# Kernel optimization log

Hardware: AMD Instinct MI355X
Metric: run time of the kernel (lower is better)

Reference implementation:

```python
import jax, jax.numpy as jnp
import numpy as np
from jax import lax

C = 32          # channel_num
DG = 8          # deformable_groups
K = 9           # 3x3 deformable kernel taps
B, H, W = 4, 192, 192


def conv2d(x, w, b, pad):
    y = lax.conv_general_dilated(x, w, (1, 1), [(pad, pad), (pad, pad)],
                                 dimension_numbers=("NCHW", "OIHW", "NCHW"))
    return y + b[None, :, None, None]


def deform_conv2d(x, offset, mask, w, b):
    """Modulated deformable conv v2, 3x3 kernel, stride 1, pad 1, dilation 1.

    x:      [B, C, H, W]
    offset: [B, 2*DG*K, H, W]  laid out as cat(o1, o2): first DG*K = dy, next = dx
    mask:   [B, DG*K, H, W]    (already sigmoided)
    w:      [Cout, C, 3, 3], b: [Cout]
    """
    Bn, Cn, Hn, Wn = x.shape
    Cg = Cn // DG
    off = offset.reshape(Bn, 2, DG, K, Hn, Wn)
    dy, dx = off[:, 0], off[:, 1]                     # [B, DG, K, H, W]
    m = mask.reshape(Bn, DG, K, Hn, Wn)

    ky = jnp.repeat(jnp.arange(3) - 1, 3).astype(x.dtype)  # [K]
    kx = jnp.tile(jnp.arange(3) - 1, 3).astype(x.dtype)    # [K]
    iy = jnp.arange(Hn, dtype=x.dtype)
    ix = jnp.arange(Wn, dtype=x.dtype)
    py = dy + ky[None, None, :, None, None] + iy[None, None, None, :, None]
    px = dx + kx[None, None, :, None, None] + ix[None, None, None, None, :]

    y0 = jnp.floor(py)
    x0 = jnp.floor(px)
    wy = py - y0    # frac weights
    wx = px - x0

    x_flat = x.reshape(Bn, DG, Cg, Hn * Wn)

    def gather(yc, xc):
        valid = (yc >= 0) & (yc < Hn) & (xc >= 0) & (xc < Wn)
        yi = jnp.clip(yc, 0, Hn - 1).astype(jnp.int32)
        xi = jnp.clip(xc, 0, Wn - 1).astype(jnp.int32)
        idx = (yi * Wn + xi).reshape(Bn, DG, 1, K * Hn * Wn)
        v = jnp.take_along_axis(x_flat, jnp.broadcast_to(idx, (Bn, DG, Cg, K * Hn * Wn)), axis=3)
        v = v.reshape(Bn, DG, Cg, K, Hn, Wn)
        return v * valid[:, :, None].astype(x.dtype)

    v00 = gather(y0, x0)
    v01 = gather(y0, x0 + 1)
    v10 = gather(y0 + 1, x0)
    v11 = gather(y0 + 1, x0 + 1)
    wyb = wy[:, :, None]  # [B, DG, 1, K, H, W]
    wxb = wx[:, :, None]
    sampled = ((1 - wyb) * (1 - wxb) * v00 + (1 - wyb) * wxb * v01
               + wyb * (1 - wxb) * v10 + wyb * wxb * v11)
    sampled = sampled * m[:, :, None]                 # modulate
    sampled = sampled.reshape(Bn, Cn, K, Hn, Wn)      # DG*Cg == C, contiguous
    out = jnp.einsum('oik,bikhw->bohw', w.reshape(w.shape[0], Cn, K), sampled)
    return out + b[None, :, None, None]


def setup_inputs() -> dict:
    key = jax.random.key(0)
    ks = jax.random.split(key, 14)
    f = lambda k, shp, s=1.0: jax.random.normal(k, shp, dtype=jnp.float32) * s
    return {
        "img_ref": f(ks[0], (B, C, H, W)),
        "img": f(ks[1], (B, C, H, W)),
        "conv1_w": f(ks[2], (C, 2 * C, 1, 1), 0.05),
        "conv1_b": f(ks[3], (C,), 0.05),
        "conv2a_w": f(ks[4], (C, C, 3, 3), 0.05),
        "conv2a_b": f(ks[5], (C,), 0.05),
        "conv2b_w": f(ks[6], (C, C, 3, 3), 0.05),
        "conv2b_b": f(ks[7], (C,), 0.05),
        "off_w": f(ks[8], (3 * DG * K, C, 3, 3), 0.01),
        "off_b": f(ks[9], (3 * DG * K,), 0.01),
        "dcn_w": f(ks[10], (C, C, 3, 3), 0.05),
        "dcn_b": f(ks[11], (C,), 0.05),
    }


def reference(img_ref, img, conv1_w, conv1_b, conv2a_w, conv2a_b,
              conv2b_w, conv2b_b, off_w, off_b, dcn_w, dcn_b):
    img_cat = conv2d(jnp.concatenate([img_ref, img], axis=1), conv1_w, conv1_b, 0)
    feat = conv2d(conv2d(img_cat, conv2a_w, conv2a_b, 1), conv2b_w, conv2b_b, 1)
    # DCNv2Pack: offsets/mask from feat, deformable sampling on img
    co = conv2d(feat, off_w, off_b, 1)                # [B, 3*DG*K, H, W]
    o1, o2, mask = jnp.split(co, 3, axis=1)
    offset = jnp.concatenate([o1, o2], axis=1)
    mask = jax.nn.sigmoid(mask)
    return deform_conv2d(img, offset, mask, dcn_w, dcn_b)
```

## Files before the change

kernel.cpp:

```cpp
#include <hip/hip_runtime.h>

#define Hc   192
#define Wc   192
#define HWc  (Hc * Wc)
#define NPIX (4 * HWc)
#define Hp   194
#define Wp   256
#define PLANE (Hp * Wp)

typedef float f32x4 __attribute__((ext_vector_type(4)));
typedef float f32x2 __attribute__((ext_vector_type(2)));
typedef __bf16 bf16x8 __attribute__((ext_vector_type(8)));
typedef unsigned short u16;
typedef unsigned int u32;

#define WF_BO    0
#define WF_B1    224
#define WF_B2A   256
#define WF_B2B   288
#define WF_BD    320
#define FR1_U    0
#define FRA_U    2048
#define FRB_U    11264
#define FRO_U    20480
#define FRD_U    84992
#define FRAG_U_TOT 94208
#define FRAG_BYTE 1408
#define T0_BYTE  (FRAG_BYTE + FRAG_U_TOT * 2)
#define T1_BYTE  (T0_BYTE + NPIX * 32 * 2)
#define IMG_BYTE (T1_BYTE + NPIX * 32 * 2)
#define IMG_SZ   ((size_t)4 * 8 * PLANE * 4 * 2)

__device__ __forceinline__ u16 f2bf(float f) {
    u32 u = __float_as_uint(f);
    u32 r = u + 0x7fffu + ((u >> 16) & 1u);
    return (u16)(r >> 16);
}
__device__ __forceinline__ float bf2f(u16 v) {
    return __uint_as_float(((u32)v) << 16);
}
__device__ __forceinline__ u32 cvtpk(float a, float b) {
    u32 r;
    asm("v_cvt_pk_bf16_f32 %0, %1, %2" : "=v"(r) : "v"(a), "v"(b));
    return r;
}
__device__ __forceinline__ f32x2 unpk(u32 h) {
    return f32x2{__uint_as_float(h << 16), __uint_as_float(h & 0xffff0000u)};
}

__global__ __launch_bounds__(256) void prep_k(
    const float* __restrict__ w1,  const float* __restrict__ b1,
    const float* __restrict__ w2a, const float* __restrict__ b2a,
    const float* __restrict__ w2b, const float* __restrict__ b2b,
    const float* __restrict__ wo,  const float* __restrict__ bo,
    const float* __restrict__ wd,  const float* __restrict__ bd,
    float* __restrict__ wsf, u16* __restrict__ frag)
{
    int i = blockIdx.x * 256 + threadIdx.x;
    if (i < 224)      { wsf[WF_BO + i]  = (i < 216) ? bo[i] : 0.f; return; }
    if (i < 256)      { wsf[WF_B1  + i - 224] = b1[i - 224];  return; }
    if (i < 288)      { wsf[WF_B2A + i - 256] = b2a[i - 256]; return; }
    if (i < 320)      { wsf[WF_B2B + i - 288] = b2b[i - 288]; return; }
    if (i < 352)      { wsf[WF_BD  + i - 320] = bd[i - 320];  return; }
    int fi = i - 352;
    if (fi < 2048) {
        int s = fi >> 10, l = (fi >> 3) & 63, j = fi & 7;
        int nt = (fi >> 9) & 1;
        int o = nt * 16 + (l & 15);
        int ci = s * 32 + ((l >> 4) << 3) + j;
        frag[FR1_U + fi] = f2bf(w1[o * 64 + ci]);
        return;
    }
    fi -= 2048;
    if (fi < 9216) {
        int s = fi / 1024, r = fi - s * 1024;
        int nt = r >> 9, l = (r >> 3) & 63, j = r & 7;
        int o = nt * 16 + (l & 15);
        int ci = ((l >> 4) << 3) + j;
        frag[FRA_U + fi] = f2bf(w2a[(o * 32 + ci) * 9 + s]);
        return;
    }
    fi -= 9216;
    if (fi < 9216) {
        int s = fi / 1024, r = fi - s * 1024;
        int nt = r >> 9, l = (r >> 3) & 63, j = r & 7;
        int o = nt * 16 + (l & 15);
        int ci = ((l >> 4) << 3) + j;
        frag[FRB_U + fi] = f2bf(w2b[(o * 32 + ci) * 9 + s]);
        return;
    }
    fi -= 9216;
    if (fi < 64512) {
        int s = fi / 7168, r = fi - s * 7168;
        int nt = r >> 9, l = (r >> 3) & 63, j = r & 7;
        int o = nt * 16 + (l & 15);
        int ci = ((l >> 4) << 3) + j;
        frag[FRO_U + fi] = f2bf((o < 216) ? wo[(o * 32 + ci) * 9 + s] : 0.f);
        return;
    }
    fi -= 64512;
    if (fi < 9216) {
        int k = fi / 1024, r = fi - k * 1024;
        int nt = r >> 9, l = (r >> 3) & 63, j = r & 7;
        int o = nt * 16 + (l & 15);
        int ci = ((l >> 4) << 3) + j;
        frag[FRD_U + fi] = f2bf(wd[o * 288 + ci * 9 + k]);
        return;
    }
}

template <int WM, int WN, int MF, int NF, int COUT, int NTILES, int KS, int MODE, bool CHL, bool DUMP>
__global__ __launch_bounds__(256) void conv_mfma_k(
    const void* __restrict__ s0v, const void* __restrict__ s1v,
    const u16* __restrict__ wfrag, const float* __restrict__ bias,
    u16* __restrict__ y, u16* __restrict__ dump)
{
    constexpr int M_BLK = WM * MF * 16;
    constexpr int ITERS = M_BLK / 64;
    const int tid = threadIdx.x, lane = tid & 63, wv = tid >> 6;
    const int wm = wv / WN, wn = wv % WN;
    const int m0 = blockIdx.x * M_BLK;
    const int b = m0 / HWc, hwb = m0 - b * HWc;
    const int rm = wm * MF * 16, cn = wn * NF * 16;

    __shared__ uint4 At4[M_BLK * 4];

    int pxA[ITERS], hA[ITERS], wA[ITERS], kgA[ITERS];
#pragma unroll
    for (int it = 0; it < ITERS; ++it) {
        int st = it * 256 + tid;
        int rowl = ((st >> 6) << 4) | (st & 15);
        kgA[it] = (st >> 4) & 3;
        pxA[it] = rowl;
        int hwp = hwb + rowl;
        hA[it] = hwp / Wc;
        wA[it] = hwp - hA[it] * Wc;
    }

    f32x4 acc[MF][NF];
#pragma unroll
    for (int mf = 0; mf < MF; ++mf)
#pragma unroll
        for (int nf = 0; nf < NF; ++nf)
            acc[mf][nf] = f32x4{0.f, 0.f, 0.f, 0.f};

    const u16* srcB = (const u16*)s0v;
    const float* f0 = (const float*)s0v;
    const float* f1 = (const float*)s1v;

    for (int s = 0; s < KS; ++s) {
        if (MODE == 1) {
            int dy = s / 3 - 1, dx = s - (s / 3) * 3 - 1;
            int d = dy * Wc + dx;
#pragma unroll
            for (int it = 0; it < ITERS; ++it) {
                bool valid = ((unsigned)(hA[it] + dy) < (unsigned)Hc) &&
                             ((unsigned)(wA[it] + dx) < (unsigned)Wc);
                uint4 v = {0u, 0u, 0u, 0u};
                if (valid)
                    v = *(const uint4*)(srcB + ((size_t)(m0 + pxA[it] + d)) * 32 + kgA[it] * 8);
                At4[it * 256 + tid] = v;
            }
        } else {
            const float* fs = (s == 0) ? f0 : f1;
#pragma unroll
            for (int it = 0; it < ITERS; ++it) {
                const float* pl = fs + ((size_t)b * 32 + kgA[it] * 8) * HWc + (hwb + pxA[it]);
                u32 p0, p1, p2, p3;
                {
                    u32 a0 = f2bf(pl[0 * HWc]), a1 = f2bf(pl[1 * HWc]);
                    u32 a2 = f2bf(pl[2 * HWc]), a3 = f2bf(pl[3 * HWc]);
                    u32 a4 = f2bf(pl[4 * HWc]), a5 = f2bf(pl[5 * HWc]);
                    u32 a6 = f2bf(pl[6 * HWc]), a7 = f2bf(pl[7 * HWc]);
                    p0 = a0 | (a1 << 16); p1 = a2 | (a3 << 16);
                    p2 = a4 | (a5 << 16); p3 = a6 | (a7 << 16);
                }
                uint4 v = {p0, p1, p2, p3};
                if (DUMP && s == 1) {
                    size_t base = (((size_t)(b * 8 + kgA[it] * 2)) * PLANE
                                   + (size_t)(hA[it] + 1) * Wp + (wA[it] + 1)) * 4;
                    *(uint2*)(dump + base) = uint2{p0, p1};
                    *(uint2*)(dump + base + (size_t)PLANE * 4) = uint2{p2, p3};
                }
                At4[it * 256 + tid] = v;
            }
        }
        __syncthreads();

        bf16x8 aF[MF];
#pragma unroll
        for (int mf = 0; mf < MF; ++mf)
            aF[mf] = __builtin_bit_cast(bf16x8, At4[((rm >> 4) + mf) * 64 + lane]);
#pragma unroll
        for (int nf = 0; nf < NF; ++nf) {
            bf16x8 bF = __builtin_bit_cast(
                bf16x8,
                *(const uint4*)(wfrag + (((size_t)s * NTILES + wn * NF + nf) * 64 + lane) * 8));
#pragma unroll
            for (int mf = 0; mf < MF; ++mf)
                acc[mf][nf] = __builtin_amdgcn_mfma_f32_16x16x32_bf16(aF[mf], bF, acc[mf][nf], 0, 0, 0);
        }
        __syncthreads();
    }

#pragma unroll
    for (int nf = 0; nf < NF; ++nf) {
        int o = cn + nf * 16 + (lane & 15);
        float bs = bias[o];
#pragma unroll
        for (int mf = 0; mf < MF; ++mf) {
#pragma unroll
            for (int r = 0; r < 4; ++r) {
                int m = m0 + rm + mf * 16 + ((lane >> 4) << 2) + r;
                float val = acc[mf][nf][r] + bs;
                y[(size_t)m * COUT + o] = f2bf(val);
            }
        }
    }
}

__global__ __launch_bounds__(256, 4) void offdcn_k(
    const u16* __restrict__ t0,
    const u16* __restrict__ imgp,
    const u16* __restrict__ wfragO,
    const u16* __restrict__ wfragD,
    const float* __restrict__ biasO,
    const float* __restrict__ biasD,
    float* __restrict__ out)
{
    const int tid = threadIdx.x, lane = tid & 63, wv = tid >> 6;
    const int bid = blockIdx.x;
    const int swz = (bid & 7) * 288 + (bid >> 3);
    const int m0 = swz * 64;
    const int b = m0 / HWc, hwb = m0 - b * HWc;
    const int h0 = hwb / Wc, w0 = hwb - h0 * Wc;

    __shared__ u16 pool[224 * 66];

    {
        u16* xt = pool;
#pragma unroll
        for (int it = 0; it < 4; ++it) {
            int t = it * 256 + tid;
            if (t < 792) {
                int s = t >> 2, c = t & 3;
                int ry = s / 66, cx = s - ry * 66;
                int row = h0 + ry - 1, col = w0 + cx - 1;
                uint4 v = {0u, 0u, 0u, 0u};
                if (((unsigned)row < (unsigned)Hc) && ((unsigned)col < (unsigned)Wc))
                    v = *(const uint4*)(t0 + ((size_t)(b * HWc + row * Wc + col)) * 32 + c * 8);
                *(uint4*)(xt + (size_t)t * 8) = v;
            }
        }
    }
    __syncthreads();

    const int wm = wv >> 1, wn = wv & 1;
    const int rm = wm * 32, cn = wn * 112;
    f32x4 acc[2][7];
#pragma unroll
    for (int mf = 0; mf < 2; ++mf)
#pragma unroll
        for (int nf = 0; nf < 7; ++nf)
            acc[mf][nf] = f32x4{0.f, 0.f, 0.f, 0.f};
    {
        const u16* xt = pool;
        const int r0 = rm + (lane & 15);
        const int kg8 = (lane >> 4) * 8;
#pragma unroll
        for (int kyi = 0; kyi < 3; ++kyi) {
#pragma unroll
            for (int kxi = 0; kxi < 3; ++kxi) {
                const int s9 = kyi * 3 + kxi;
                bf16x8 aF0 = __builtin_bit_cast(bf16x8,
                    *(const uint4*)(xt + (size_t)(kyi * 66 + r0 + kxi) * 32 + kg8));
                bf16x8 aF1 = __builtin_bit_cast(bf16x8,
                    *(const uint4*)(xt + (size_t)(kyi * 66 + r0 + 16 + kxi) * 32 + kg8));
#pragma unroll
                for (int nf = 0; nf < 7; ++nf) {
                    bf16x8 bF = __builtin_bit_cast(
                        bf16x8,
                        *(const uint4*)(wfragO + (((size_t)s9 * 14 + wn * 7 + nf) * 64 + lane) * 8));
                    acc[0][nf] = __builtin_amdgcn_mfma_f32_16x16x32_bf16(aF0, bF, acc[0][nf], 0, 0, 0);
                    acc[1][nf] = __builtin_amdgcn_mfma_f32_16x16x32_bf16(aF1, bF, acc[1][nf], 0, 0, 0);
                }
            }
        }
    }
    __syncthreads();

    u16* co_s = pool;
#pragma unroll
    for (int nf = 0; nf < 7; ++nf) {
        const int o = cn + nf * 16 + (lane & 15);
        const float bs = biasO[o];
        const bool sig = (o >= 144);
#pragma unroll
        for (int mf = 0; mf < 2; ++mf) {
            const int mb = rm + mf * 16 + ((lane >> 4) << 2);
            float v0 = acc[mf][nf][0] + bs, v1 = acc[mf][nf][1] + bs;
            float v2 = acc[mf][nf][2] + bs, v3 = acc[mf][nf][3] + bs;
            if (sig) {
                v0 = __builtin_amdgcn_rcpf(1.f + __builtin_amdgcn_exp2f(-v0 * 1.44269504f));
                v1 = __builtin_amdgcn_rcpf(1.f + __builtin_amdgcn_exp2f(-v1 * 1.44269504f));
                v2 = __builtin_amdgcn_rcpf(1.f + __builtin_amdgcn_exp2f(-v2 * 1.44269504f));
                v3 = __builtin_amdgcn_rcpf(1.f + __builtin_amdgcn_exp2f(-v3 * 1.44269504f));
            }
            *(u32*)&co_s[o * 66 + mb]     = cvtpk(v0, v1);
            *(u32*)&co_s[o * 66 + mb + 2] = cvtpk(v2, v3);
        }
    }
    __syncthreads();

    {
        const int kg = lane >> 4;
        const int pixb = wv * 16 + (lane & 15);
        const int hw = hwb + pixb;
        const int hh = hw / Wc;
        const int wwp = hw - hh * Wc;

        f32x4 acc0 = {0.f, 0.f, 0.f, 0.f};
        f32x4 acc1 = {0.f, 0.f, 0.f, 0.f};

#pragma unroll 1
        for (int kb = 0; kb < 9; kb += 3) {
            float w4[3][2][4];
            uint2 cc[3][2][4];

#pragma unroll
            for (int t = 0; t < 3; ++t) {
                const int k = kb + t;
                const int kyi = k / 3, kxi = k - kyi * 3;
#pragma unroll
                for (int dgi = 0; dgi < 2; ++dgi) {
                    const int dg = 2 * kg + dgi;
                    const int offch = dg * 9 + k;
                    float dy = bf2f(co_s[offch * 66 + pixb]);
                    float dx = bf2f(co_s[(72 + offch) * 66 + pixb]);
                    float m  = bf2f(co_s[(144 + offch) * 66 + pixb]);

                    float py = dy + (float)(hh + kyi - 1);
                    float px = dx + (float)(wwp + kxi - 1);
                    float y0f = floorf(py), x0f = floorf(px);
                    float wy = py - y0f, wx = px - x0f;
                    int y0 = (int)y0f, x0 = (int)x0f;

                    int yA = min(max(y0 + 1, 0), 193);
                    int yB = min(max(y0 + 2, 0), 193);
                    int xA = min(max(x0 + 1, 0), 193);
                    int xB = min(max(x0 + 2, 0), 193);

                    float w1y = 1.f - wy, w1x = 1.f - wx;
                    w4[t][dgi][0] = w1y * w1x * m;
                    w4[t][dgi][1] = w1y * wx  * m;
                    w4[t][dgi][2] = wy  * w1x * m;
                    w4[t][dgi][3] = wy  * wx  * m;

                    const u16* pp = imgp + ((size_t)(b * 8 + dg)) * PLANE * 4;
                    cc[t][dgi][0] = *(const uint2*)(pp + (size_t)((yA << 8) + xA) * 4);
                    cc[t][dgi][1] = *(const uint2*)(pp + (size_t)((yA << 8) + xB) * 4);
                    cc[t][dgi][2] = *(const uint2*)(pp + (size_t)((yB << 8) + xA) * 4);
                    cc[t][dgi][3] = *(const uint2*)(pp + (size_t)((yB << 8) + xB) * 4);
                }
            }

#pragma unroll
            for (int t = 0; t < 3; ++t) {
                const int k = kb + t;
                u32 pk[4];
#pragma unroll
                for (int dgi = 0; dgi < 2; ++dgi) {
                    f32x2 sA = unpk(cc[t][dgi][0].x) * w4[t][dgi][0]
                             + unpk(cc[t][dgi][1].x) * w4[t][dgi][1]
                             + unpk(cc[t][dgi][2].x) * w4[t][dgi][2]
                             + unpk(cc[t][dgi][3].x) * w4[t][dgi][3];
                    f32x2 sB = unpk(cc[t][dgi][0].y) * w4[t][dgi][0]
                             + unpk(cc[t][dgi][1].y) * w4[t][dgi][1]
                             + unpk(cc[t][dgi][2].y) * w4[t][dgi][2]
                             + unpk(cc[t][dgi][3].y) * w4[t][dgi][3];
                    pk[dgi * 2 + 0] = cvtpk(sA.x, sA.y);
                    pk[dgi * 2 + 1] = cvtpk(sB.x, sB.y);
                }

                bf16x8 aF = __builtin_bit_cast(bf16x8, uint4{pk[0], pk[1], pk[2], pk[3]});
                bf16x8 bF0 = __builtin_bit_cast(bf16x8,
                    *(const uint4*)(wfragD + ((size_t)(k * 2 + 0) * 64 + lane) * 8));
                bf16x8 bF1 = __builtin_bit_cast(bf16x8,
                    *(const uint4*)(wfragD + ((size_t)(k * 2 + 1) * 64 + lane) * 8));
                acc0 = __builtin_amdgcn_mfma_f32_16x16x32_bf16(aF, bF0, acc0, 0, 0, 0);
                acc1 = __builtin_amdgcn_mfma_f32_16x16x32_bf16(aF, bF1, acc1, 0, 0, 0);
            }
        }

        const int hw0 = hwb + wv * 16 + ((lane >> 4) << 2);
        float* ob = out + (size_t)b * 32 * HWc;
        const int oL = lane & 15;
        const float bs0 = biasD[oL], bs1 = biasD[16 + oL];
        f32x4 o0 = {acc0[0] + bs0, acc0[1] + bs0, acc0[2] + bs0, acc0[3] + bs0};
        f32x4 o1 = {acc1[0] + bs1, acc1[1] + bs1, acc1[2] + bs1, acc1[3] + bs1};
        *(f32x4*)(ob + (size_t)oL * HWc + hw0) = o0;
        *(f32x4*)(ob + (size_t)(16 + oL) * HWc + hw0) = o1;
    }
}

extern "C" void kernel_launch(void* const* d_in, const int* in_sizes, int n_in,
                              void* d_out, int out_size, void* d_ws, size_t ws_size,
                              hipStream_t stream) {
    const float* img_ref  = (const float*)d_in[0];
    const float* img      = (const float*)d_in[1];
    const float* conv1_w  = (const float*)d_in[2];
    const float* conv1_b  = (const float*)d_in[3];
    const float* conv2a_w = (const float*)d_in[4];
    const float* conv2a_b = (const float*)d_in[5];
    const float* conv2b_w = (const float*)d_in[6];
    const float* conv2b_b = (const float*)d_in[7];
    const float* off_w    = (const float*)d_in[8];
    const float* off_b    = (const float*)d_in[9];
    const float* dcn_w    = (const float*)d_in[10];
    const float* dcn_b    = (const float*)d_in[11];

    float* wsf = (float*)d_ws;
    u16* frag = (u16*)((char*)d_ws + FRAG_BYTE);
    u16* t0   = (u16*)((char*)d_ws + T0_BYTE);
    u16* t1   = (u16*)((char*)d_ws + T1_BYTE);
    u16* imgp = (u16*)((char*)d_ws + IMG_BYTE);
    float* out = (float*)d_out;

    hipMemsetAsync(imgp, 0, IMG_SZ, stream);

    prep_k<<<370, 256, 0, stream>>>(conv1_w, conv1_b, conv2a_w, conv2a_b,
                                    conv2b_w, conv2b_b, off_w, off_b,
                                    dcn_w, dcn_b, wsf, frag);

    conv_mfma_k<4, 1, 2, 2, 32, 2, 2, 0, true, true>
        <<<NPIX / 128, 256, 0, stream>>>(img_ref, img, frag + FR1_U, wsf + WF_B1, t0, imgp);

    conv_mfma_k<4, 1, 2, 2, 32, 2, 9, 1, true, false>
        <<<NPIX / 128, 256, 0, stream>>>(t0, nullptr, frag + FRA_U, wsf + WF_B2A, t1, nullptr);

    conv_mfma_k<4, 1, 2, 2, 32, 2, 9, 1, true, false>
        <<<NPIX / 128, 256, 0, stream>>>(t1, nullptr, frag + FRB_U, wsf + WF_B2B, t0, nullptr);

    offdcn_k<<<NPIX / 64, 256, 0, stream>>>(t0, imgp, frag + FRO_U, frag + FRD_U,
                                            wsf + WF_BO, wsf + WF_BD, out);
}
```

Baseline: 111.8 us.

## Replace generic 3x3 conv with halo-tiled LDS kernel and swizzle block order

The templated MFMA conv is split into a dedicated 1x1 kernel and a new 3x3 kernel. The 3x3 kernel loads a 3-row halo tile of 64-pixel rows into shared memory once, then reads all nine taps from it, instead of reloading the A tile from global memory for each tap with a sync per tap. Block indices are swizzled by gridDim across all kernels, and the deformable gather uses 32-bit offset arithmetic. The trade-off is smaller 64-pixel blocks and some redundant halo loads.

```diff
diff --git a/kernel.cpp b/kernel.cpp
--- a/kernel.cpp
+++ b/kernel.cpp
@@ -109,25 +109,24 @@
     }
 }
 
-template <int WM, int WN, int MF, int NF, int COUT, int NTILES, int KS, int MODE, bool CHL, bool DUMP>
-__global__ __launch_bounds__(256) void conv_mfma_k(
-    const void* __restrict__ s0v, const void* __restrict__ s1v,
+__global__ __launch_bounds__(256) void conv1x1_mfma_k(
+    const float* __restrict__ f0, const float* __restrict__ f1,
     const u16* __restrict__ wfrag, const float* __restrict__ bias,
     u16* __restrict__ y, u16* __restrict__ dump)
 {
-    constexpr int M_BLK = WM * MF * 16;
-    constexpr int ITERS = M_BLK / 64;
+    constexpr int M_BLK = 128;
     const int tid = threadIdx.x, lane = tid & 63, wv = tid >> 6;
-    const int wm = wv / WN, wn = wv % WN;
-    const int m0 = blockIdx.x * M_BLK;
+    const int bid = blockIdx.x;
+    const int swz = (bid & 7) * (gridDim.x >> 3) + (bid >> 3);
+    const int m0 = swz * M_BLK;
     const int b = m0 / HWc, hwb = m0 - b * HWc;
-    const int rm = wm * MF * 16, cn = wn * NF * 16;
-
-    __shared__ uint4 At4[M_BLK * 4];
-
-    int pxA[ITERS], hA[ITERS], wA[ITERS], kgA[ITERS];
-#pragma unroll
-    for (int it = 0; it < ITERS; ++it) {
+    const int rm = wv * 32;
+
+    __shared__ uint4 At4[512];
+
+    int pxA[2], hA[2], wA[2], kgA[2];
+#pragma unroll
+    for (int it = 0; it < 2; ++it) {
         int st = it * 256 + tid;
         int rowl = ((st >> 6) << 4) | (st & 15);
         kgA[it] = (st >> 4) & 3;
@@ -137,85 +136,125 @@
         wA[it] = hwp - hA[it] * Wc;
     }
 
-    f32x4 acc[MF][NF];
-#pragma unroll
-    for (int mf = 0; mf < MF; ++mf)
-#pragma unroll
-        for (int nf = 0; nf < NF; ++nf)
+    f32x4 acc[2][2];
+#pragma unroll
+    for (int mf = 0; mf < 2; ++mf)
+#pragma unroll
+        for (int nf = 0; nf < 2; ++nf)
             acc[mf][nf] = f32x4{0.f, 0.f, 0.f, 0.f};
 
-    const u16* srcB = (const u16*)s0v;
-    const float* f0 = (const float*)s0v;
-    const float* f1 = (const float*)s1v;
-
-    for (int s = 0; s < KS; ++s) {
-        if (MODE == 1) {
-            int dy = s / 3 - 1, dx = s - (s / 3) * 3 - 1;
-            int d = dy * Wc + dx;
-#pragma unroll
-            for (int it = 0; it < ITERS; ++it) {
-                bool valid = ((unsigned)(hA[it] + dy) < (unsigned)Hc) &&
-                             ((unsigned)(wA[it] + dx) < (unsigned)Wc);
-                uint4 v = {0u, 0u, 0u, 0u};
-                if (valid)
-                    v = *(const uint4*)(srcB + ((size_t)(m0 + pxA[it] + d)) * 32 + kgA[it] * 8);
-                At4[it * 256 + tid] = v;
-            }
-        } else {
-            const float* fs = (s == 0) ? f0 : f1;
-#pragma unroll
-            for (int it = 0; it < ITERS; ++it) {
-                const float* pl = fs + ((size_t)b * 32 + kgA[it] * 8) * HWc + (hwb + pxA[it]);
-                u32 p0, p1, p2, p3;
-                {
-                    u32 a0 = f2bf(pl[0 * HWc]), a1 = f2bf(pl[1 * HWc]);
-                    u32 a2 = f2bf(pl[2 * HWc]), a3 = f2bf(pl[3 * HWc]);
-                    u32 a4 = f2bf(pl[4 * HWc]), a5 = f2bf(pl[5 * HWc]);
-                    u32 a6 = f2bf(pl[6 * HWc]), a7 = f2bf(pl[7 * HWc]);
-                    p0 = a0 | (a1 << 16); p1 = a2 | (a3 << 16);
-                    p2 = a4 | (a5 << 16); p3 = a6 | (a7 << 16);
-                }
-                uint4 v = {p0, p1, p2, p3};
-                if (DUMP && s == 1) {
-                    size_t base = (((size_t)(b * 8 + kgA[it] * 2)) * PLANE
-                                   + (size_t)(hA[it] + 1) * Wp + (wA[it] + 1)) * 4;
-                    *(uint2*)(dump + base) = uint2{p0, p1};
-                    *(uint2*)(dump + base + (size_t)PLANE * 4) = uint2{p2, p3};
-                }
-                At4[it * 256 + tid] = v;
-            }
+    for (int s = 0; s < 2; ++s) {
+        const float* fs = (s == 0) ? f0 : f1;
+#pragma unroll
+        for (int it = 0; it < 2; ++it) {
+            const float* pl = fs + ((size_t)b * 32 + kgA[it] * 8) * HWc + (hwb + pxA[it]);
+            u32 p0, p1, p2, p3;
+            {
+                u32 a0 = f2bf(pl[0 * HWc]), a1 = f2bf(pl[1 * HWc]);
+                u32 a2 = f2bf(pl[2 * HWc]), a3 = f2bf(pl[3 * HWc]);
+                u32 a4 = f2bf(pl[4 * HWc]), a5 = f2bf(pl[5 * HWc]);
+                u32 a6 = f2bf(pl[6 * HWc]), a7 = f2bf(pl[7 * HWc]);
+                p0 = a0 | (a1 << 16); p1 = a2 | (a3 << 16);
+                p2 = a4 | (a5 << 16); p3 = a6 | (a7 << 16);
+            }
+            uint4 v = {p0, p1, p2, p3};
+            if (s == 1) {
+                size_t base = (((size_t)(b * 8 + kgA[it] * 2)) * PLANE
+                               + (size_t)(hA[it] + 1) * Wp + (wA[it] + 1)) * 4;
+                *(uint2*)(dump + base) = uint2{p0, p1};
+                *(uint2*)(dump + base + (size_t)PLANE * 4) = uint2{p2, p3};
+            }
+            At4[it * 256 + tid] = v;
         }
         __syncthreads();
 
-        bf16x8 aF[MF];
-#pragma unroll
-        for (int mf = 0; mf < MF; ++mf)
+        bf16x8 aF[2];
+#pragma unroll
+        for (int mf = 0; mf < 2; ++mf)
             aF[mf] = __builtin_bit_cast(bf16x8, At4[((rm >> 4) + mf) * 64 + lane]);
 #pragma unroll
-        for (int nf = 0; nf < NF; ++nf) {
+        for (int nf = 0; nf < 2; ++nf) {
             bf16x8 bF = __builtin_bit_cast(
-                bf16x8,
-                *(const uint4*)(wfrag + (((size_t)s * NTILES + wn * NF + nf) * 64 + lane) * 8));
-#pragma unroll
-            for (int mf = 0; mf < MF; ++mf)
+                bf16x8, *(const uint4*)(wfrag + (((size_t)s * 2 + nf) * 64 + lane) * 8));
+#pragma unroll
+            for (int mf = 0; mf < 2; ++mf)
                 acc[mf][nf] = __builtin_amdgcn_mfma_f32_16x16x32_bf16(aF[mf], bF, acc[mf][nf], 0, 0, 0);
         }
         __syncthreads();
     }
 
 #pragma unroll
-    for (int nf = 0; nf < NF; ++nf) {
-        int o = cn + nf * 16 + (lane & 15);
+    for (int nf = 0; nf < 2; ++nf) {
+        int o = nf * 16 + (lane & 15);
         float bs = bias[o];
 #pragma unroll
-        for (int mf = 0; mf < MF; ++mf) {
+        for (int mf = 0; mf < 2; ++mf) {
 #pragma unroll
             for (int r = 0; r < 4; ++r) {
                 int m = m0 + rm + mf * 16 + ((lane >> 4) << 2) + r;
-                float val = acc[mf][nf][r] + bs;
-                y[(size_t)m * COUT + o] = f2bf(val);
-            }
-        }
+                y[(size_t)m * 32 + o] = f2bf(acc[mf][nf][r] + bs);
+            }
+        }
+    }
+}
+
+__global__ __launch_bounds__(256, 4) void conv3x3h_k(
+    const u16* __restrict__ src,
+    const u16* __restrict__ wfrag,
+    const float* __restrict__ bias,
+    u16* __restrict__ dst)
+{
+    const int tid = threadIdx.x, lane = tid & 63, wv = tid >> 6;
+    const int bid = blockIdx.x;
+    const int swz = (bid & 7) * (gridDim.x >> 3) + (bid >> 3);
+    const int m0 = swz * 64;
+    const int b = m0 / HWc, hwb = m0 - b * HWc;
+    const int h0 = hwb / Wc, w0 = hwb - h0 * Wc;
+
+    __shared__ u16 xt[198 * 32];
+
+#pragma unroll
+    for (int it = 0; it < 4; ++it) {
+        int t = it * 256 + tid;
+        if (t < 792) {
+            int s = t >> 2, c = t & 3;
+            int ry = s / 66, cx = s - ry * 66;
+            int row = h0 + ry - 1, col = w0 + cx - 1;
+            uint4 v = {0u, 0u, 0u, 0u};
+            if (((unsigned)row < (unsigned)Hc) && ((unsigned)col < (unsigned)Wc))
+                v = *(const uint4*)(src + ((size_t)(b * HWc + row * Wc + col)) * 32 + c * 8);
+            *(uint4*)(xt + (size_t)t * 8) = v;
+        }
+    }
+    __syncthreads();
+
+    f32x4 acc0 = {0.f, 0.f, 0.f, 0.f};
+    f32x4 acc1 = {0.f, 0.f, 0.f, 0.f};
+    const int r0 = wv * 16 + (lane & 15);
+    const int kg8 = (lane >> 4) * 8;
+#pragma unroll
+    for (int kyi = 0; kyi < 3; ++kyi) {
+#pragma unroll
+        for (int kxi = 0; kxi < 3; ++kxi) {
+            const int s9 = kyi * 3 + kxi;
+            bf16x8 aF = __builtin_bit_cast(bf16x8,
+                *(const uint4*)(xt + (size_t)(kyi * 66 + r0 + kxi) * 32 + kg8));
+            bf16x8 bF0 = __builtin_bit_cast(bf16x8,
+                *(const uint4*)(wfrag + (((size_t)s9 * 2 + 0) * 64 + lane) * 8));
+            bf16x8 bF1 = __builtin_bit_cast(bf16x8,
+                *(const uint4*)(wfrag + (((size_t)s9 * 2 + 1) * 64 + lane) * 8));
+            acc0 = __builtin_amdgcn_mfma_f32_16x16x32_bf16(aF, bF0, acc0, 0, 0, 0);
+            acc1 = __builtin_amdgcn_mfma_f32_16x16x32_bf16(aF, bF1, acc1, 0, 0, 0);
+        }
+    }
+
+    const int oL = lane & 15;
+    const float bs0 = bias[oL], bs1 = bias[16 + oL];
+    u16* dp = dst + (size_t)(m0 + wv * 16 + ((lane >> 4) << 2)) * 32;
+#pragma unroll
+    for (int r = 0; r < 4; ++r) {
+        dp[r * 32 + oL]      = f2bf(acc0[r] + bs0);
+        dp[r * 32 + 16 + oL] = f2bf(acc1[r] + bs1);
     }
 }
 
@@ -230,7 +269,7 @@
 {
     const int tid = threadIdx.x, lane = tid & 63, wv = tid >> 6;
     const int bid = blockIdx.x;
-    const int swz = (bid & 7) * 288 + (bid >> 3);
+    const int swz = (bid & 7) * (gridDim.x >> 3) + (bid >> 3);
     const int m0 = swz * 64;
     const int b = m0 / HWc, hwb = m0 - b * HWc;
     const int h0 = hwb / Wc, w0 = hwb - h0 * Wc;
@@ -318,6 +357,12 @@
         const int hw = hwb + pixb;
         const int hh = hw / Wc;
         const int wwp = hw - hh * Wc;
+        const float fh = (float)(hh - 1);
+        const float fw = (float)(wwp - 1);
+
+        const u16* gb = imgp + (size_t)b * 8 * PLANE * 4;
+        const u32 dgp[2] = {(u32)((2 * kg + 0) * (PLANE * 4)),
+                            (u32)((2 * kg + 1) * (PLANE * 4))};
 
         f32x4 acc0 = {0.f, 0.f, 0.f, 0.f};
         f32x4 acc1 = {0.f, 0.f, 0.f, 0.f};
@@ -333,14 +378,13 @@
                 const int kyi = k / 3, kxi = k - kyi * 3;
 #pragma unroll
                 for (int dgi = 0; dgi < 2; ++dgi) {
-                    const int dg = 2 * kg + dgi;
-                    const int offch = dg * 9 + k;
+                    const int offch = (2 * kg + dgi) * 9 + k;
                     float dy = bf2f(co_s[offch * 66 + pixb]);
                     float dx = bf2f(co_s[(72 + offch) * 66 + pixb]);
                     float m  = bf2f(co_s[(144 + offch) * 66 + pixb]);
 
-                    float py = dy + (float)(hh + kyi - 1);
-                    float px = dx + (float)(wwp + kxi - 1);
+                    float py = dy + (fh + (float)kyi);
+                    float px = dx + (fw + (float)kxi);
                     float y0f = floorf(py), x0f = floorf(px);
                     float wy = py - y0f, wx = px - x0f;
                     int y0 = (int)y0f, x0 = (int)x0f;
@@ -356,11 +400,13 @@
                     w4[t][dgi][2] = wy  * w1x * m;
                     w4[t][dgi][3] = wy  * wx  * m;
 
-                    const u16* pp = imgp + ((size_t)(b * 8 + dg)) * PLANE * 4;
-                    cc[t][dgi][0] = *(const uint2*)(pp + (size_t)((yA << 8) + xA) * 4);
-                    cc[t][dgi][1] = *(const uint2*)(pp + (size_t)((yA << 8) + xB) * 4);
-                    cc[t][dgi][2] = *(const uint2*)(pp + (size_t)((yB << 8) + xA) * 4);
-                    cc[t][dgi][3] = *(const uint2*)(pp + (size_t)((yB << 8) + xB) * 4);
+                    u32 rA = dgp[dgi] + ((u32)yA << 10);
+                    u32 rB = dgp[dgi] + ((u32)yB << 10);
+                    u32 xA4 = (u32)xA << 2, xB4 = (u32)xB << 2;
+                    cc[t][dgi][0] = *(const uint2*)(gb + (rA + xA4));
+                    cc[t][dgi][1] = *(const uint2*)(gb + (rA + xB4));
+                    cc[t][dgi][2] = *(const uint2*)(gb + (rB + xA4));
+                    cc[t][dgi][3] = *(const uint2*)(gb + (rB + xB4));
                 }
             }
 
@@ -432,14 +478,12 @@
                                     conv2b_w, conv2b_b, off_w, off_b,
                                     dcn_w, dcn_b, wsf, frag);
 
-    conv_mfma_k<4, 1, 2, 2, 32, 2, 2, 0, true, true>
-        <<<NPIX / 128, 256, 0, stream>>>(img_ref, img, frag + FR1_U, wsf + WF_B1, t0, imgp);
-
-    conv_mfma_k<4, 1, 2, 2, 32, 2, 9, 1, true, false>
-        <<<NPIX / 128, 256, 0, stream>>>(t0, nullptr, frag + FRA_U, wsf + WF_B2A, t1, nullptr);
-
-    conv_mfma_k<4, 1, 2, 2, 32, 2, 9, 1, true, false>
-        <<<NPIX / 128, 256, 0, stream>>>(t1, nullptr, frag + FRB_U, wsf + WF_B2B, t0, nullptr);
+    conv1x1_mfma_k<<<NPIX / 128, 256, 0, stream>>>(
+        img_ref, img, frag + FR1_U, wsf + WF_B1, t0, imgp);
+
+    conv3x3h_k<<<NPIX / 64, 256, 0, stream>>>(t0, frag + FRA_U, wsf + WF_B2A, t1);
+
+    conv3x3h_k<<<NPIX / 64, 256, 0, stream>>>(t1, frag + FRB_U, wsf + WF_B2B, t0);
 
     offdcn_k<<<NPIX / 64, 256, 0, stream>>>(t0, imgp, frag + FRO_U, frag + FRD_U,
                                             wsf + WF_BO, wsf + WF_BD, out);
```

After: 107.4 us. 3.9% less time.
